# Performance work log

Measured on AMD Instinct MI355X. Metric: run time of the kernel, lower is better.

The kernel has to match this reference:

```python
import jax, jax.numpy as jnp
import numpy as np


def setup_inputs() -> dict:
    key = jax.random.key(0)
    kq, kk, kv = jax.random.split(key, 3)
    B, H, S, D = 4, 16, 2048, 64
    Q = jax.random.normal(kq, (B, H, S, D), dtype=jnp.float32)
    K = jax.random.normal(kk, (B, H, S, D), dtype=jnp.float32)
    V = jax.random.normal(kv, (B, H, S, D), dtype=jnp.float32)
    return {"Q": Q, "K": K, "V": V}


def reference(Q, K, V):
    # Faithful to the source: scale = d**(-2); scores = (Q @ K^T) / scale
    # i.e. scores are MULTIPLIED by d^2 (quirk of the original module).
    d = K.shape[-1]
    scale = jnp.asarray(d, Q.dtype) ** (-2)
    scores = jnp.einsum('bhqd,bhkd->bhqk', Q, K) / scale  # [B,H,S,S]
    attn = jax.nn.softmax(scores, axis=-1)
    out = jnp.einsum('bhqk,bhkd->bhqd', attn, V)
    return out
```

## Files before the change

### kernel.cpp

```cpp
#include <hip/hip_runtime.h>
#include <math.h>


#define S_LEN 2048
#define D_DIM 64
#define NH 64
#define BM 128
#define BN 64
#define QTILES (S_LEN / BM)
#define KTILES (S_LEN / BN)

typedef unsigned short u16;
typedef unsigned int u32;
typedef _Float16 f16;
typedef __attribute__((ext_vector_type(4))) _Float16 f16x4;
typedef __attribute__((ext_vector_type(8))) _Float16 f16x8;
typedef __attribute__((ext_vector_type(2))) __fp16 fp16x2;
typedef __attribute__((ext_vector_type(4))) float f32x4;

#define SC_FULL (4096.0f * 1.4426950408889634f)
#define QSCALE (SC_FULL / 64.0f)
#define KSCALE 64.0f

union f16cv { f16 h; u16 u; };
union pk4 { fp16x2 h2[2]; f16x4 v; };

__device__ __forceinline__ void split2h(float a, u16& hi, u16& lo) {
  f16cv ch, cl;
  ch.h = (f16)a;
  float r = a - (float)ch.h;
  cl.h = (f16)r;
  hi = ch.u; lo = cl.u;
}

__device__ __forceinline__ int swz(int row, int chunk) {
  return (row << 6) + ((chunk ^ (row & 7)) << 3);
}

__global__ void prep_kernel(const float* __restrict__ K, const float* __restrict__ V,
                            u16* __restrict__ Kh, u16* __restrict__ Km,
                            u16* __restrict__ Vt) {
  if (blockIdx.x < 8192) {
    size_t i4 = ((size_t)blockIdx.x * 256 + threadIdx.x) * 4;
    float4 v = *(const float4*)(K + i4);
    u16 h0, l0, h1, l1, h2, l2, h3, l3;
    split2h(v.x * KSCALE, h0, l0);
    split2h(v.y * KSCALE, h1, l1);
    split2h(v.z * KSCALE, h2, l2);
    split2h(v.w * KSCALE, h3, l3);
    *(uint2*)(Kh + i4) = make_uint2((u32)h0 | ((u32)h1 << 16), (u32)h2 | ((u32)h3 << 16));
    *(uint2*)(Km + i4) = make_uint2((u32)l0 | ((u32)l1 << 16), (u32)l2 | ((u32)l3 << 16));
  } else {
    __shared__ float Vf[64 * 65];
    const int idx = blockIdx.x - 8192;
    const int kt = idx & 31, h = idx >> 5;
    const int tid = threadIdx.x;
    const float* V0 = V + ((size_t)h * S_LEN + kt * 64) * 64;
    const int tx = tid & 15, ty = tid >> 4;
#pragma unroll
    for (int p = 0; p < 4; ++p) {
      int r = ty + 16 * p;
      float4 v = *(const float4*)(V0 + r * 64 + tx * 4);
      Vf[r * 65 + 4 * tx + 0] = v.x;
      Vf[r * 65 + 4 * tx + 1] = v.y;
      Vf[r * 65 + 4 * tx + 2] = v.z;
      Vf[r * 65 + 4 * tx + 3] = v.w;
    }
    __syncthreads();
    const int ch = tid & 7, dr = tid >> 3;
#pragma unroll
    for (int p = 0; p < 2; ++p) {
      int d = dr + 32 * p;
      u32 w[4];
#pragma unroll
      for (int i = 0; i < 4; ++i) {
        f16cv a, b;
        a.h = (f16)Vf[(8 * ch + 2 * i) * 65 + d];
        b.h = (f16)Vf[(8 * ch + 2 * i + 1) * 65 + d];
        w[i] = (u32)a.u | ((u32)b.u << 16);
      }
      size_t o = ((size_t)h * 64 + d) * S_LEN + (size_t)kt * 64 + 8 * ch;
      *(uint4*)(Vt + o) = make_uint4(w[0], w[1], w[2], w[3]);
    }
  }
}

#define K0_B 0
#define K1_B 4096
#define VT_B 8192
#define LDS_USH 12288

__global__ __launch_bounds__(256, 3)
void attn_mfma_f16(const float* __restrict__ Q, const u16* __restrict__ Kh,
                   const u16* __restrict__ Km, const u16* __restrict__ Vt,
                   float* __restrict__ O) {
  __shared__ __align__(16) u16 lds[LDS_USH];

  const int tid = threadIdx.x;
  const int lane = tid & 63;
  const int wv = tid >> 6;
  const int c = lane & 15;
  const int g = lane >> 4;
  const int h = blockIdx.x;
  const int qtile = blockIdx.y;

  f16x8 aqh[2][2], aqm[2][2];
#pragma unroll
  for (int m = 0; m < 2; ++m) {
    int qrow = qtile * BM + wv * 32 + m * 16 + c;
    const float* qp = Q + ((size_t)h * S_LEN + qrow) * 64 + g * 8;
#pragma unroll
    for (int ks = 0; ks < 2; ++ks) {
      float4 a = *(const float4*)(qp + ks * 32);
      float4 b = *(const float4*)(qp + ks * 32 + 4);
      float v[8] = {a.x, a.y, a.z, a.w, b.x, b.y, b.z, b.w};
      f16x8 hi, lo;
#pragma unroll
      for (int e = 0; e < 8; ++e) {
        float q = v[e] * QSCALE;
        f16 qh = (f16)q;
        hi[e] = qh;
        lo[e] = (f16)(q - (float)qh);
      }
      aqh[m][ks] = hi; aqm[m][ks] = lo;
    }
  }

  f32x4 Oacc[2][4];
  float mrow[2] = {-INFINITY, -INFINITY};
  float lrow[2] = {0.f, 0.f};
#pragma unroll
  for (int m = 0; m < 2; ++m)
#pragma unroll
    for (int t = 0; t < 4; ++t) Oacc[m][t] = (f32x4){0.f, 0.f, 0.f, 0.f};

  const int srow = tid >> 2;
  const int c0 = tid & 3;
  const int d0a = swz(srow, c0), d0b = swz(srow, c0 + 4);
  const size_t gKbase = ((size_t)h * S_LEN + srow) * 64 + c0 * 8;
  const size_t gVbase = ((size_t)h * 64 + srow) * S_LEN + c0 * 8;

  uint4 rk0a = *(const uint4*)(Kh + gKbase);
  uint4 rk0b = *(const uint4*)(Kh + gKbase + 32);
  uint4 rk1a = *(const uint4*)(Km + gKbase);
  uint4 rk1b = *(const uint4*)(Km + gKbase + 32);
  uint4 rva  = *(const uint4*)(Vt + gVbase);
  uint4 rvb  = *(const uint4*)(Vt + gVbase + 32);

  for (int kt = 0; kt < KTILES; ++kt) {
    __syncthreads();
    *(uint4*)&lds[K0_B + d0a] = rk0a;
    *(uint4*)&lds[K0_B + d0b] = rk0b;
    *(uint4*)&lds[K1_B + d0a] = rk1a;
    *(uint4*)&lds[K1_B + d0b] = rk1b;
    *(uint4*)&lds[VT_B + d0a] = rva;
    *(uint4*)&lds[VT_B + d0b] = rvb;
    __syncthreads();

    if (kt + 1 < KTILES) {
      size_t gK = gKbase + (size_t)(kt + 1) * BN * 64;
      size_t gV = gVbase + (size_t)(kt + 1) * BN;
      rk0a = *(const uint4*)(Kh + gK);
      rk0b = *(const uint4*)(Kh + gK + 32);
      rk1a = *(const uint4*)(Km + gK);
      rk1b = *(const uint4*)(Km + gK + 32);
      rva  = *(const uint4*)(Vt + gV);
      rvb  = *(const uint4*)(Vt + gV + 32);
    }

    f32x4 S[2][4];
#pragma unroll
    for (int m = 0; m < 2; ++m)
#pragma unroll
      for (int t = 0; t < 4; ++t) S[m][t] = (f32x4){0.f, 0.f, 0.f, 0.f};
    __builtin_amdgcn_s_setprio(1);
#pragma unroll
    for (int ks = 0; ks < 2; ++ks) {
#pragma unroll
      for (int t = 0; t < 4; ++t) {
        int off = swz(16 * t + c, g + 4 * ks);
        f16x8 bh = *(const f16x8*)&lds[K0_B + off];
        f16x8 bm = *(const f16x8*)&lds[K1_B + off];
#pragma unroll
        for (int m = 0; m < 2; ++m) {
          S[m][t] = __builtin_amdgcn_mfma_f32_16x16x32_f16(bh, aqh[m][ks], S[m][t], 0, 0, 0);
          S[m][t] = __builtin_amdgcn_mfma_f32_16x16x32_f16(bm, aqh[m][ks], S[m][t], 0, 0, 0);
          S[m][t] = __builtin_amdgcn_mfma_f32_16x16x32_f16(bh, aqm[m][ks], S[m][t], 0, 0, 0);
        }
      }
    }
    __builtin_amdgcn_s_setprio(0);

    f16x4 ap[2][4];
#pragma unroll
    for (int m = 0; m < 2; ++m) {
      float x0 = fmaxf(fmaxf(S[m][0][0], S[m][0][1]), fmaxf(S[m][0][2], S[m][0][3]));
      float x1 = fmaxf(fmaxf(S[m][1][0], S[m][1][1]), fmaxf(S[m][1][2], S[m][1][3]));
      float x2 = fmaxf(fmaxf(S[m][2][0], S[m][2][1]), fmaxf(S[m][2][2], S[m][2][3]));
      float x3 = fmaxf(fmaxf(S[m][3][0], S[m][3][1]), fmaxf(S[m][3][2], S[m][3][3]));
      float mx = fmaxf(fmaxf(x0, x1), fmaxf(x2, x3));
      mx = fmaxf(mx, __shfl_xor(mx, 16));
      mx = fmaxf(mx, __shfl_xor(mx, 32));
      float mnew = fmaxf(mrow[m], mx);
      float a = exp2f(mrow[m] - mnew);
      mrow[m] = mnew;
      float ps = 0.f;
#pragma unroll
      for (int t = 0; t < 4; ++t) {
        float p0 = exp2f(S[m][t][0] - mnew);
        float p1 = exp2f(S[m][t][1] - mnew);
        float p2 = exp2f(S[m][t][2] - mnew);
        float p3 = exp2f(S[m][t][3] - mnew);
        ps += (p0 + p1) + (p2 + p3);
        pk4 w;
        w.h2[0] = __builtin_amdgcn_cvt_pkrtz(p0, p1);
        w.h2[1] = __builtin_amdgcn_cvt_pkrtz(p2, p3);
        ap[m][t] = w.v;
      }
      lrow[m] = lrow[m] * a + ps;
#pragma unroll
      for (int nt = 0; nt < 4; ++nt)
#pragma unroll
        for (int r = 0; r < 4; ++r) Oacc[m][nt][r] *= a;
    }

    __builtin_amdgcn_s_setprio(1);
#pragma unroll
    for (int nt = 0; nt < 4; ++nt) {
      const int rv = 16 * nt + c;
      const int rb = VT_B + rv * 64 + 4 * (g & 1);
      const int r7 = rv & 7;
#pragma unroll
      for (int t = 0; t < 4; ++t) {
        f16x4 bv = *(const f16x4*)&lds[rb + (((2 * t + (g >> 1)) ^ r7) << 3)];
#pragma unroll
        for (int m = 0; m < 2; ++m)
          Oacc[m][nt] = __builtin_amdgcn_mfma_f32_16x16x16f16(bv, ap[m][t], Oacc[m][nt], 0, 0, 0);
      }
    }
    __builtin_amdgcn_s_setprio(0);
  }

#pragma unroll
  for (int m = 0; m < 2; ++m) {
    float l = lrow[m];
    l += __shfl_xor(l, 16);
    l += __shfl_xor(l, 32);
    float linv = 1.0f / l;
    int q = qtile * BM + wv * 32 + m * 16 + c;
    float* op = O + ((size_t)h * S_LEN + q) * 64 + 4 * g;
#pragma unroll
    for (int nt = 0; nt < 4; ++nt) {
      float4 o;
      o.x = Oacc[m][nt][0] * linv;
      o.y = Oacc[m][nt][1] * linv;
      o.z = Oacc[m][nt][2] * linv;
      o.w = Oacc[m][nt][3] * linv;
      *(float4*)(op + 16 * nt) = o;
    }
  }
}

#define LSTR 68
__global__ __launch_bounds__(256, 2)
void attn_fp32_kernel(const float* __restrict__ Q, const float* __restrict__ K,
                      const float* __restrict__ V, float* __restrict__ O) {
  __shared__ float Qs[64][LSTR];
  __shared__ float Ks[64][LSTR];
  __shared__ float Vs[64][LSTR];
  __shared__ float Ps[64][LSTR];
  const int tid = threadIdx.x;
  const int tx = tid & 15, ty = tid >> 4;
  const int qtile = blockIdx.x, head = blockIdx.y;
  const long hoff = (long)head * S_LEN * D_DIM;
  const float* Qp = Q + hoff + (long)qtile * 64 * D_DIM;
  const float* Kp = K + hoff;
  const float* Vp = V + hoff;
  float* Op = O + hoff + (long)qtile * 64 * D_DIM;
  {
    const int cc = tx * 4;
#pragma unroll
    for (int p = 0; p < 4; ++p) {
      const int r = ty + p * 16;
      *(float4*)(&Qs[r][cc]) = *(const float4*)(Qp + r * D_DIM + cc);
    }
  }
  float m_i[4], l_i[4];
  float4 o_acc[4];
#pragma unroll
  for (int i = 0; i < 4; ++i) {
    m_i[i] = -INFINITY; l_i[i] = 0.0f;
    o_acc[i] = make_float4(0.f, 0.f, 0.f, 0.f);
  }
  const float SCALE = 4096.0f;
  const float LOG2E = 1.4426950408889634f;
  for (int kt = 0; kt < S_LEN / 64; ++kt) {
    {
      const int cc = tx * 4;
      const float* Kt = Kp + kt * 64 * D_DIM;
      const float* Vv = Vp + kt * 64 * D_DIM;
#pragma unroll
      for (int p = 0; p < 4; ++p) {
        const int r = ty + p * 16;
        *(float4*)(&Ks[r][cc]) = *(const float4*)(Kt + r * D_DIM + cc);
        *(float4*)(&Vs[r][cc]) = *(const float4*)(Vv + r * D_DIM + cc);
      }
    }
    __syncthreads();
    float s[4][4];
#pragma unroll
    for (int i = 0; i < 4; ++i)
#pragma unroll
      for (int j = 0; j < 4; ++j) s[i][j] = 0.0f;
#pragma unroll
    for (int d = 0; d < D_DIM; d += 4) {
      float4 q4[4], k4[4];
#pragma unroll
      for (int i = 0; i < 4; ++i) q4[i] = *(const float4*)(&Qs[ty * 4 + i][d]);
#pragma unroll
      for (int j = 0; j < 4; ++j) k4[j] = *(const float4*)(&Ks[tx + 16 * j][d]);
#pragma unroll
      for (int i = 0; i < 4; ++i)
#pragma unroll
        for (int j = 0; j < 4; ++j) {
          s[i][j] += q4[i].x * k4[j].x; s[i][j] += q4[i].y * k4[j].y;
          s[i][j] += q4[i].z * k4[j].z; s[i][j] += q4[i].w * k4[j].w;
        }
    }
#pragma unroll
    for (int i = 0; i < 4; ++i) {
#pragma unroll
      for (int j = 0; j < 4; ++j) s[i][j] *= SCALE;
      float rm = fmaxf(fmaxf(s[i][0], s[i][1]), fmaxf(s[i][2], s[i][3]));
#pragma unroll
      for (int off = 8; off >= 1; off >>= 1) rm = fmaxf(rm, __shfl_xor(rm, off));
      const float mnew = fmaxf(m_i[i], rm);
      const float alpha = exp2f((m_i[i] - mnew) * LOG2E);
      float rs = 0.0f;
#pragma unroll
      for (int j = 0; j < 4; ++j) {
        const float p = exp2f((s[i][j] - mnew) * LOG2E);
        s[i][j] = p; rs += p;
      }
#pragma unroll
      for (int off = 8; off >= 1; off >>= 1) rs += __shfl_xor(rs, off);
      l_i[i] = l_i[i] * alpha + rs;
      m_i[i] = mnew;
      o_acc[i].x *= alpha; o_acc[i].y *= alpha; o_acc[i].z *= alpha; o_acc[i].w *= alpha;
      const int mm = ty * 4 + i;
      Ps[mm][tx] = s[i][0]; Ps[mm][tx + 16] = s[i][1];
      Ps[mm][tx + 32] = s[i][2]; Ps[mm][tx + 48] = s[i][3];
    }
    __syncthreads();
#pragma unroll
    for (int k = 0; k < 64; k += 4) {
      float4 p4[4], v4[4];
#pragma unroll
      for (int i = 0; i < 4; ++i) p4[i] = *(const float4*)(&Ps[ty * 4 + i][k]);
#pragma unroll
      for (int kk = 0; kk < 4; ++kk) v4[kk] = *(const float4*)(&Vs[k + kk][tx * 4]);
#pragma unroll
      for (int i = 0; i < 4; ++i) {
        o_acc[i].x += p4[i].x * v4[0].x + p4[i].y * v4[1].x + p4[i].z * v4[2].x + p4[i].w * v4[3].x;
        o_acc[i].y += p4[i].x * v4[0].y + p4[i].y * v4[1].y + p4[i].z * v4[2].y + p4[i].w * v4[3].y;
        o_acc[i].z += p4[i].x * v4[0].z + p4[i].y * v4[1].z + p4[i].z * v4[2].z + p4[i].w * v4[3].z;
        o_acc[i].w += p4[i].x * v4[0].w + p4[i].y * v4[1].w + p4[i].z * v4[2].w + p4[i].w * v4[3].w;
      }
    }
    __syncthreads();
  }
#pragma unroll
  for (int i = 0; i < 4; ++i) {
    const float inv = 1.0f / l_i[i];
    o_acc[i].x *= inv; o_acc[i].y *= inv; o_acc[i].z *= inv; o_acc[i].w *= inv;
    *(float4*)(Op + (ty * 4 + i) * D_DIM + tx * 4) = o_acc[i];
  }
}

extern "C" void kernel_launch(void* const* d_in, const int* in_sizes, int n_in,
                              void* d_out, int out_size, void* d_ws, size_t ws_size,
                              hipStream_t stream) {
  const float* Q = (const float*)d_in[0];
  const float* K = (const float*)d_in[1];
  const float* V = (const float*)d_in[2];
  float* O = (float*)d_out;

  const size_t P = (size_t)NH * S_LEN * D_DIM;
  const size_t need = 3 * P * sizeof(u16);

  if (ws_size >= need) {
    u16* w = (u16*)d_ws;
    u16 *Kh = w, *Km = w + P, *Vt = w + 2 * P;
    prep_kernel<<<8192 + 2048, 256, 0, stream>>>(K, V, Kh, Km, Vt);
    attn_mfma_f16<<<dim3(NH, QTILES), 256, 0, stream>>>(Q, Kh, Km, Vt, O);
  } else {
    attn_fp32_kernel<<<dim3(S_LEN / 64, NH), 256, 0, stream>>>(Q, K, V, O);
  }
}
```

Before: 306.0 us.

## Shrink query tile to 64 rows with one 16-row slab per wave

Halves the query tile per block from 128 to 64 rows, so each of the four waves handles a single 16-row slab instead of two. This doubles the grid size and cuts register use per thread, aiming for more blocks in flight and better latency hiding. In exchange, each K/V tile loaded into LDS is reused by half as many query rows, which doubles global and LDS traffic per unit of compute.

```diff
diff --git a/kernel.cpp b/kernel.cpp
--- a/kernel.cpp
+++ b/kernel.cpp
@@ -5,7 +5,7 @@
 #define S_LEN 2048
 #define D_DIM 64
 #define NH 64
-#define BM 128
+#define BM 64
 #define BN 64
 #define QTILES (S_LEN / BM)
 #define KTILES (S_LEN / BN)
@@ -104,10 +104,9 @@
   const int h = blockIdx.x;
   const int qtile = blockIdx.y;
 
-  f16x8 aqh[2][2], aqm[2][2];
-#pragma unroll
-  for (int m = 0; m < 2; ++m) {
-    int qrow = qtile * BM + wv * 32 + m * 16 + c;
+  f16x8 aqh[2], aqm[2];
+  {
+    int qrow = qtile * BM + wv * 16 + c;
     const float* qp = Q + ((size_t)h * S_LEN + qrow) * 64 + g * 8;
 #pragma unroll
     for (int ks = 0; ks < 2; ++ks) {
@@ -122,17 +121,15 @@
         hi[e] = qh;
         lo[e] = (f16)(q - (float)qh);
       }
-      aqh[m][ks] = hi; aqm[m][ks] = lo;
-    }
-  }
-
-  f32x4 Oacc[2][4];
-  float mrow[2] = {-INFINITY, -INFINITY};
-  float lrow[2] = {0.f, 0.f};
-#pragma unroll
-  for (int m = 0; m < 2; ++m)
-#pragma unroll
-    for (int t = 0; t < 4; ++t) Oacc[m][t] = (f32x4){0.f, 0.f, 0.f, 0.f};
+      aqh[ks] = hi; aqm[ks] = lo;
+    }
+  }
+
+  f32x4 Oacc[4];
+  float mrow = -INFINITY;
+  float lrow = 0.f;
+#pragma unroll
+  for (int t = 0; t < 4; ++t) Oacc[t] = (f32x4){0.f, 0.f, 0.f, 0.f};
 
   const int srow = tid >> 2;
   const int c0 = tid & 3;
@@ -168,11 +165,9 @@
       rvb  = *(const uint4*)(Vt + gV + 32);
     }
 
-    f32x4 S[2][4];
-#pragma unroll
-    for (int m = 0; m < 2; ++m)
-#pragma unroll
-      for (int t = 0; t < 4; ++t) S[m][t] = (f32x4){0.f, 0.f, 0.f, 0.f};
+    f32x4 S[4];
+#pragma unroll
+    for (int t = 0; t < 4; ++t) S[t] = (f32x4){0.f, 0.f, 0.f, 0.f};
     __builtin_amdgcn_s_setprio(1);
 #pragma unroll
     for (int ks = 0; ks < 2; ++ks) {
@@ -181,47 +176,43 @@
         int off = swz(16 * t + c, g + 4 * ks);
         f16x8 bh = *(const f16x8*)&lds[K0_B + off];
         f16x8 bm = *(const f16x8*)&lds[K1_B + off];
-#pragma unroll
-        for (int m = 0; m < 2; ++m) {
-          S[m][t] = __builtin_amdgcn_mfma_f32_16x16x32_f16(bh, aqh[m][ks], S[m][t], 0, 0, 0);
-          S[m][t] = __builtin_amdgcn_mfma_f32_16x16x32_f16(bm, aqh[m][ks], S[m][t], 0, 0, 0);
-          S[m][t] = __builtin_amdgcn_mfma_f32_16x16x32_f16(bh, aqm[m][ks], S[m][t], 0, 0, 0);
-        }
+        S[t] = __builtin_amdgcn_mfma_f32_16x16x32_f16(bh, aqh[ks], S[t], 0, 0, 0);
+        S[t] = __builtin_amdgcn_mfma_f32_16x16x32_f16(bm, aqh[ks], S[t], 0, 0, 0);
+        S[t] = __builtin_amdgcn_mfma_f32_16x16x32_f16(bh, aqm[ks], S[t], 0, 0, 0);
       }
     }
     __builtin_amdgcn_s_setprio(0);
 
-    f16x4 ap[2][4];
-#pragma unroll
-    for (int m = 0; m < 2; ++m) {
-      float x0 = fmaxf(fmaxf(S[m][0][0], S[m][0][1]), fmaxf(S[m][0][2], S[m][0][3]));
-      float x1 = fmaxf(fmaxf(S[m][1][0], S[m][1][1]), fmaxf(S[m][1][2], S[m][1][3]));
-      float x2 = fmaxf(fmaxf(S[m][2][0], S[m][2][1]), fmaxf(S[m][2][2], S[m][2][3]));
-      float x3 = fmaxf(fmaxf(S[m][3][0], S[m][3][1]), fmaxf(S[m][3][2], S[m][3][3]));
+    f16x4 ap[4];
+    {
+      float x0 = fmaxf(fmaxf(S[0][0], S[0][1]), fmaxf(S[0][2], S[0][3]));
+      float x1 = fmaxf(fmaxf(S[1][0], S[1][1]), fmaxf(S[1][2], S[1][3]));
+      float x2 = fmaxf(fmaxf(S[2][0], S[2][1]), fmaxf(S[2][2], S[2][3]));
+      float x3 = fmaxf(fmaxf(S[3][0], S[3][1]), fmaxf(S[3][2], S[3][3]));
       float mx = fmaxf(fmaxf(x0, x1), fmaxf(x2, x3));
       mx = fmaxf(mx, __shfl_xor(mx, 16));
       mx = fmaxf(mx, __shfl_xor(mx, 32));
-      float mnew = fmaxf(mrow[m], mx);
-      float a = exp2f(mrow[m] - mnew);
-      mrow[m] = mnew;
+      float mnew = fmaxf(mrow, mx);
+      float a = exp2f(mrow - mnew);
+      mrow = mnew;
       float ps = 0.f;
 #pragma unroll
       for (int t = 0; t < 4; ++t) {
-        float p0 = exp2f(S[m][t][0] - mnew);
-        float p1 = exp2f(S[m][t][1] - mnew);
-        float p2 = exp2f(S[m][t][2] - mnew);
-        float p3 = exp2f(S[m][t][3] - mnew);
+        float p0 = exp2f(S[t][0] - mnew);
+        float p1 = exp2f(S[t][1] - mnew);
+        float p2 = exp2f(S[t][2] - mnew);
+        float p3 = exp2f(S[t][3] - mnew);
         ps += (p0 + p1) + (p2 + p3);
         pk4 w;
         w.h2[0] = __builtin_amdgcn_cvt_pkrtz(p0, p1);
         w.h2[1] = __builtin_amdgcn_cvt_pkrtz(p2, p3);
-        ap[m][t] = w.v;
-      }
-      lrow[m] = lrow[m] * a + ps;
+        ap[t] = w.v;
+      }
+      lrow = lrow * a + ps;
 #pragma unroll
       for (int nt = 0; nt < 4; ++nt)
 #pragma unroll
-        for (int r = 0; r < 4; ++r) Oacc[m][nt][r] *= a;
+        for (int r = 0; r < 4; ++r) Oacc[nt][r] *= a;
     }
 
     __builtin_amdgcn_s_setprio(1);
@@ -233,29 +224,26 @@
 #pragma unroll
       for (int t = 0; t < 4; ++t) {
         f16x4 bv = *(const f16x4*)&lds[rb + (((2 * t + (g >> 1)) ^ r7) << 3)];
-#pragma unroll
-        for (int m = 0; m < 2; ++m)
-          Oacc[m][nt] = __builtin_amdgcn_mfma_f32_16x16x16f16(bv, ap[m][t], Oacc[m][nt], 0, 0, 0);
+        Oacc[nt] = __builtin_amdgcn_mfma_f32_16x16x16f16(bv, ap[t], Oacc[nt], 0, 0, 0);
       }
     }
     __builtin_amdgcn_s_setprio(0);
   }
 
-#pragma unroll
-  for (int m = 0; m < 2; ++m) {
-    float l = lrow[m];
+  {
+    float l = lrow;
     l += __shfl_xor(l, 16);
     l += __shfl_xor(l, 32);
     float linv = 1.0f / l;
-    int q = qtile * BM + wv * 32 + m * 16 + c;
+    int q = qtile * BM + wv * 16 + c;
     float* op = O + ((size_t)h * S_LEN + q) * 64 + 4 * g;
 #pragma unroll
     for (int nt = 0; nt < 4; ++nt) {
       float4 o;
-      o.x = Oacc[m][nt][0] * linv;
-      o.y = Oacc[m][nt][1] * linv;
-      o.z = Oacc[m][nt][2] * linv;
-      o.w = Oacc[m][nt][3] * linv;
+      o.x = Oacc[nt][0] * linv;
+      o.y = Oacc[nt][1] * linv;
+      o.z = Oacc[nt][2] * linv;
+      o.w = Oacc[nt][3] * linv;
       *(float4*)(op + 16 * nt) = o;
     }
   }
```

Result: slower. 312.6 us (+2.2%).

## Double-buffer K/V tiles in LDS and skip rescaling when row max barely changes

Applied to the files above, without the earlier changes.

Switches the LDS staging to two buffers so the next tile is written while the current one is consumed, which drops one of the two barriers per iteration. Global prefetch now runs two tiles ahead, and the load mapping changes to 8 threads per row for contiguous 128-byte rows. The online softmax skips the exp2 and accumulator rescale unless the wave-wide max rises by more than 8 (log2 units), so probabilities can grow up to 256 before being cast to f16. This trades more LDS per block, which may reduce occupancy, and more live registers for fewer syncs and less rescaling ALU work.

```diff
diff --git a/kernel.cpp b/kernel.cpp
--- a/kernel.cpp
+++ b/kernel.cpp
@@ -88,7 +88,8 @@
 #define K0_B 0
 #define K1_B 4096
 #define VT_B 8192
-#define LDS_USH 12288
+#define BUF_USH 12288
+#define LDS_USH 24576
 
 __global__ __launch_bounds__(256, 3)
 void attn_mfma_f16(const float* __restrict__ Q, const u16* __restrict__ Kh,
@@ -134,39 +135,43 @@
 #pragma unroll
     for (int t = 0; t < 4; ++t) Oacc[m][t] = (f32x4){0.f, 0.f, 0.f, 0.f};
 
-  const int srow = tid >> 2;
-  const int c0 = tid & 3;
-  const int d0a = swz(srow, c0), d0b = swz(srow, c0 + 4);
-  const size_t gKbase = ((size_t)h * S_LEN + srow) * 64 + c0 * 8;
-  const size_t gVbase = ((size_t)h * 64 + srow) * S_LEN + c0 * 8;
-
-  uint4 rk0a = *(const uint4*)(Kh + gKbase);
-  uint4 rk0b = *(const uint4*)(Kh + gKbase + 32);
-  uint4 rk1a = *(const uint4*)(Km + gKbase);
-  uint4 rk1b = *(const uint4*)(Km + gKbase + 32);
-  uint4 rva  = *(const uint4*)(Vt + gVbase);
-  uint4 rvb  = *(const uint4*)(Vt + gVbase + 32);
+  const int rs = tid >> 3;
+  const int cl = tid & 7;
+  const int d0 = swz(rs, cl);
+  const size_t gK0 = ((size_t)h * S_LEN + rs) * 64 + cl * 8;
+  const size_t gV0 = ((size_t)h * 64 + rs) * S_LEN + cl * 8;
+
+  uint4 rk0a, rk0b, rk1a, rk1b, rva, rvb;
+  auto load6 = [&](int kt) {
+    size_t gK = gK0 + (size_t)kt * 4096;
+    size_t gV = gV0 + (size_t)kt * 64;
+    rk0a = *(const uint4*)(Kh + gK);
+    rk0b = *(const uint4*)(Kh + gK + 2048);
+    rk1a = *(const uint4*)(Km + gK);
+    rk1b = *(const uint4*)(Km + gK + 2048);
+    rva  = *(const uint4*)(Vt + gV);
+    rvb  = *(const uint4*)(Vt + gV + (size_t)32 * S_LEN);
+  };
+  auto write6 = [&](int b) {
+    u16* lb = lds + b * BUF_USH;
+    *(uint4*)&lb[K0_B + d0] = rk0a;
+    *(uint4*)&lb[K0_B + d0 + 2048] = rk0b;
+    *(uint4*)&lb[K1_B + d0] = rk1a;
+    *(uint4*)&lb[K1_B + d0 + 2048] = rk1b;
+    *(uint4*)&lb[VT_B + d0] = rva;
+    *(uint4*)&lb[VT_B + d0 + 2048] = rvb;
+  };
+
+  load6(0);
+  write6(0);
+  load6(1);
+  __syncthreads();
 
   for (int kt = 0; kt < KTILES; ++kt) {
-    __syncthreads();
-    *(uint4*)&lds[K0_B + d0a] = rk0a;
-    *(uint4*)&lds[K0_B + d0b] = rk0b;
-    *(uint4*)&lds[K1_B + d0a] = rk1a;
-    *(uint4*)&lds[K1_B + d0b] = rk1b;
-    *(uint4*)&lds[VT_B + d0a] = rva;
-    *(uint4*)&lds[VT_B + d0b] = rvb;
-    __syncthreads();
-
-    if (kt + 1 < KTILES) {
-      size_t gK = gKbase + (size_t)(kt + 1) * BN * 64;
-      size_t gV = gVbase + (size_t)(kt + 1) * BN;
-      rk0a = *(const uint4*)(Kh + gK);
-      rk0b = *(const uint4*)(Kh + gK + 32);
-      rk1a = *(const uint4*)(Km + gK);
-      rk1b = *(const uint4*)(Km + gK + 32);
-      rva  = *(const uint4*)(Vt + gV);
-      rvb  = *(const uint4*)(Vt + gV + 32);
-    }
+    const int cb = (kt & 1) * BUF_USH;
+
+    if (kt + 1 < KTILES) write6((kt + 1) & 1);
+    if (kt + 2 < KTILES) load6(kt + 2);
 
     f32x4 S[2][4];
 #pragma unroll
@@ -178,7 +183,7 @@
     for (int ks = 0; ks < 2; ++ks) {
 #pragma unroll
       for (int t = 0; t < 4; ++t) {
-        int off = swz(16 * t + c, g + 4 * ks);
+        int off = cb + swz(16 * t + c, g + 4 * ks);
         f16x8 bh = *(const f16x8*)&lds[K0_B + off];
         f16x8 bm = *(const f16x8*)&lds[K1_B + off];
 #pragma unroll
@@ -201,34 +206,37 @@
       float mx = fmaxf(fmaxf(x0, x1), fmaxf(x2, x3));
       mx = fmaxf(mx, __shfl_xor(mx, 16));
       mx = fmaxf(mx, __shfl_xor(mx, 32));
-      float mnew = fmaxf(mrow[m], mx);
-      float a = exp2f(mrow[m] - mnew);
-      mrow[m] = mnew;
+      if (!__all(mx - mrow[m] <= 8.0f)) {
+        float mnew = fmaxf(mrow[m], mx);
+        float a = exp2f(mrow[m] - mnew);
+        mrow[m] = mnew;
+        lrow[m] *= a;
+#pragma unroll
+        for (int nt = 0; nt < 4; ++nt)
+#pragma unroll
+          for (int r = 0; r < 4; ++r) Oacc[m][nt][r] *= a;
+      }
       float ps = 0.f;
 #pragma unroll
       for (int t = 0; t < 4; ++t) {
-        float p0 = exp2f(S[m][t][0] - mnew);
-        float p1 = exp2f(S[m][t][1] - mnew);
-        float p2 = exp2f(S[m][t][2] - mnew);
-        float p3 = exp2f(S[m][t][3] - mnew);
+        float p0 = exp2f(S[m][t][0] - mrow[m]);
+        float p1 = exp2f(S[m][t][1] - mrow[m]);
+        float p2 = exp2f(S[m][t][2] - mrow[m]);
+        float p3 = exp2f(S[m][t][3] - mrow[m]);
         ps += (p0 + p1) + (p2 + p3);
         pk4 w;
         w.h2[0] = __builtin_amdgcn_cvt_pkrtz(p0, p1);
         w.h2[1] = __builtin_amdgcn_cvt_pkrtz(p2, p3);
         ap[m][t] = w.v;
       }
-      lrow[m] = lrow[m] * a + ps;
-#pragma unroll
-      for (int nt = 0; nt < 4; ++nt)
-#pragma unroll
-        for (int r = 0; r < 4; ++r) Oacc[m][nt][r] *= a;
+      lrow[m] += ps;
     }
 
     __builtin_amdgcn_s_setprio(1);
 #pragma unroll
     for (int nt = 0; nt < 4; ++nt) {
       const int rv = 16 * nt + c;
-      const int rb = VT_B + rv * 64 + 4 * (g & 1);
+      const int rb = cb + VT_B + rv * 64 + 4 * (g & 1);
       const int r7 = rv & 7;
 #pragma unroll
       for (int t = 0; t < 4; ++t) {
@@ -239,6 +247,8 @@
       }
     }
     __builtin_amdgcn_s_setprio(0);
+
+    __syncthreads();
   }
 
 #pragma unroll
```

After: 305.2 us. No clear change (-0.3%).
